# Kernel tuning notes

Measured on AMD Instinct MI355X. Metric: run time of the kernel, lower is better.

The kernel has to match this reference:

```python
import jax, jax.numpy as jnp
import numpy as np

N = 200_000      # total nodes
E = 3_200_000    # directed edges
F = 128          # input features
G = 2_000        # graphs in batch
SIZES = (128, 128, 128, 128, 128, 64)
K = 2            # TAGConv hops
EPS = 1e-5


def setup_inputs() -> dict:
    key = jax.random.key(0)
    ks = jax.random.split(key, 12)
    x = jax.random.normal(ks[0], (N, F), jnp.float32)
    edge_index = jax.random.randint(ks[1], (2, E), 0, N, dtype=jnp.int32).astype(jnp.int64)
    segment_ids = jnp.sort(jax.random.randint(ks[2], (N,), 0, G, dtype=jnp.int32)).astype(jnp.int64)
    conv_W = jax.random.normal(ks[3], (5, (K + 1) * 128, 128), jnp.float32) * 0.05
    conv_W_last = jax.random.normal(ks[4], ((K + 1) * 128, 64), jnp.float32) * 0.05
    bn_gamma = jnp.ones((5, 128), jnp.float32)
    bn_beta = jnp.zeros((5, 128), jnp.float32)
    bn_gamma_last = jnp.ones((64,), jnp.float32)
    bn_beta_last = jnp.zeros((64,), jnp.float32)
    agg_bn_gamma = jnp.ones((4,), jnp.float32)
    agg_bn_beta = jnp.zeros((4,), jnp.float32)
    agg_W = jax.random.normal(ks[5], (64, 4 * 64), jnp.float32) * 0.05
    agg_b = jnp.zeros((64,), jnp.float32)
    out_W = jax.random.normal(ks[6], (1, 64), jnp.float32) * 0.05
    out_b = jnp.zeros((1,), jnp.float32)
    return dict(x=x, edge_index=edge_index, segment_ids=segment_ids, conv_W=conv_W,
                conv_W_last=conv_W_last, bn_gamma=bn_gamma, bn_beta=bn_beta,
                bn_gamma_last=bn_gamma_last, bn_beta_last=bn_beta_last,
                agg_bn_gamma=agg_bn_gamma, agg_bn_beta=agg_bn_beta,
                agg_W=agg_W, agg_b=agg_b, out_W=out_W, out_b=out_b)


def _forward(x, edge_index, segment_ids, conv_W, conv_W_last, bn_gamma, bn_beta,
             bn_gamma_last, bn_beta_last, agg_bn_gamma, agg_bn_beta,
             agg_W, agg_b, out_W, out_b):
    src, dst = edge_index[0], edge_index[1]
    deg = jax.ops.segment_sum(jnp.ones((E,), x.dtype), dst, num_segments=N)
    norm = jnp.where(deg > 0, jax.lax.rsqrt(jnp.maximum(deg, 1.0)), 0.0)[:, None]  # D^{-1/2}

    def prop(h):  # h: [N, d] -> D^{-1/2} A D^{-1/2} h
        return norm * jax.ops.segment_sum((h * norm)[src], dst, num_segments=N)

    def tagconv(h, W):  # concat of A_norm^k h for k=0..K, then linear (no bias; BN follows)
        hs = [h]
        for _ in range(K):
            hs.append(prop(hs[-1]))
        return jnp.concatenate(hs, axis=-1) @ W

    def bn(h, g, b):  # training-mode batchnorm over nodes
        m = h.mean(0)
        v = h.var(0)
        return (h - m) * jax.lax.rsqrt(v + EPS) * g + b

    outs = []
    h = x
    for l in range(len(SIZES)):
        if l < 5:
            W, g, b = conv_W[l], bn_gamma[l], bn_beta[l]
        else:
            W, g, b = conv_W_last, bn_gamma_last, bn_beta_last
        h = jax.nn.relu(bn(tagconv(h, W), g, b))
        if l >= 2 and SIZES[l] == SIZES[l - 2]:  # skip connection
            h = h + outs[l - 2]
        outs.append(h)

    # ragged pooling: (max, min, mean, std) per graph
    counts = jax.ops.segment_sum(jnp.ones((N,), h.dtype), segment_ids, num_segments=G)[:, None]
    s = jax.ops.segment_sum(h, segment_ids, num_segments=G)
    mean = s / jnp.maximum(counts, 1.0)
    ssq = jax.ops.segment_sum(h * h, segment_ids, num_segments=G)
    var = (ssq - counts * mean * mean) / jnp.maximum(counts - 1.0, 1.0)  # unbiased like th.std
    std = jnp.sqrt(jnp.maximum(var, 0.0))
    mx = jax.ops.segment_max(h, segment_ids, num_segments=G)
    mn = jax.ops.segment_min(h, segment_ids, num_segments=G)
    pooled = jnp.stack([mx, mn, mean, std], axis=1)  # [G, 4, 64]

    # aggregation BatchNorm1d over the 4 pooling channels (stats over graphs x feat)
    m = pooled.mean(axis=(0, 2))
    v = pooled.var(axis=(0, 2))
    pooled = (pooled - m[None, :, None]) * jax.lax.rsqrt(v + EPS)[None, :, None] \
             * agg_bn_gamma[None, :, None] + agg_bn_beta[None, :, None]

    flat = pooled.reshape(G, 4 * SIZES[-1])
    hg = flat @ agg_W.T + agg_b           # aggregation Linear(256 -> 64)
    return hg @ out_W.T + out_b           # output Linear(64 -> 1), shape [G, 1]


def reference(x, edge_index, segment_ids, conv_W, conv_W_last, bn_gamma, bn_beta,
              bn_gamma_last, bn_beta_last, agg_bn_gamma, agg_bn_beta,
              agg_W, agg_b, out_W, out_b):
    return _forward(x, edge_index, segment_ids, conv_W, conv_W_last, bn_gamma, bn_beta,
                    bn_gamma_last, bn_beta_last, agg_bn_gamma, agg_bn_beta,
                    agg_W, agg_b, out_W, out_b)
```

## Files before the change

kernel.cpp:

```cpp
#include <hip/hip_runtime.h>
#include <cstddef>
#include <cstdint>

#define N_NODES  200000
#define N_EDGES  3200000
#define N_GRAPHS 2000
#define BN_EPS   1e-5f
#define NB       391
#define BSH      9
#define CHUNK    16384

typedef unsigned int   u32;
typedef unsigned short u16;

using short8   = __attribute__((ext_vector_type(8))) short;
using floatx16 = __attribute__((ext_vector_type(16))) float;

__device__ __forceinline__ float bflo(u32 v) { union {u32 i; float f;} c; c.i = v << 16; return c.f; }
__device__ __forceinline__ float bfhi(u32 v) { union {u32 i; float f;} c; c.i = v & 0xffff0000u; return c.f; }
__device__ __forceinline__ float bf1(u16 v)  { union {u32 i; float f;} c; c.i = ((u32)v) << 16; return c.f; }
__device__ __forceinline__ u32 f2bf(float f) {
    union {float f; u32 i;} c; c.f = f;
    return (c.i + 0x7fffu + ((c.i >> 16) & 1u)) >> 16;
}
__device__ __forceinline__ u32 pack2(float a, float b) { return f2bf(a) | (f2bf(b) << 16); }

__global__ void x2bf_kernel(const float* __restrict__ x, u16* __restrict__ xb, int total4) {
    for (int i = blockIdx.x * 256 + threadIdx.x; i < total4; i += gridDim.x * 256) {
        float4 v = ((const float4*)x)[i];
        uint2 o; o.x = pack2(v.x, v.y); o.y = pack2(v.z, v.w);
        ((uint2*)xb)[i] = o;
    }
}

__global__ void wpack_kernel(const float* __restrict__ W, u16* __restrict__ whi,
                             u16* __restrict__ wlo, int K, int DOUT) {
    int tid = blockIdx.x * 256 + threadIdx.x;
    if (tid >= K * DOUT) return;
    int k = tid / DOUT, nn = tid % DOUT;
    float w = W[tid];
    u16 hi = (u16)f2bf(w);
    float rem = w - bf1(hi);
    u16 lo = (u16)f2bf(rem);
    int dst = (k >> 6) * DOUT * 64 + nn * 64 + (k & 63);
    whi[dst] = hi;
    wlo[dst] = lo;
}

__global__ __launch_bounds__(256)
void bucket_hist(const int* __restrict__ edst, int* __restrict__ bcnt, int e) {
    __shared__ int h[NB];
    for (int t = threadIdx.x; t < NB; t += 256) h[t] = 0;
    __syncthreads();
    int base = blockIdx.x * CHUNK;
    int end  = min(base + CHUNK, e);
    for (int i = base + threadIdx.x; i < end; i += 256)
        atomicAdd(&h[edst[i] >> BSH], 1);
    __syncthreads();
    for (int t = threadIdx.x; t < NB; t += 256)
        if (h[t]) atomicAdd(&bcnt[t], h[t]);
}

__global__ void bucket_scan(const int* __restrict__ bcnt, int* __restrict__ bbase,
                            int* __restrict__ bcur) {
    __shared__ int ls[512];
    int t = threadIdx.x;
    int v = (t < NB) ? bcnt[t] : 0;
    ls[t] = v;
    __syncthreads();
    for (int off = 1; off < 512; off <<= 1) {
        int a = (t >= off) ? ls[t - off] : 0;
        __syncthreads();
        ls[t] += a;
        __syncthreads();
    }
    if (t <= NB) {
        int excl = ls[t] - v;
        bbase[t] = excl;
        if (t < NB) bcur[t] = excl;
    }
}

__global__ __launch_bounds__(256)
void bucket_scatter(const int* __restrict__ esrc, const int* __restrict__ edst,
                    int* __restrict__ bcur, uint2* __restrict__ esorted, int e) {
    __shared__ int h[NB], lbase[NB], lcur[NB];
    for (int t = threadIdx.x; t < NB; t += 256) { h[t] = 0; lcur[t] = 0; }
    __syncthreads();
    int base = blockIdx.x * CHUNK;
    int end  = min(base + CHUNK, e);
    for (int i = base + threadIdx.x; i < end; i += 256)
        atomicAdd(&h[edst[i] >> BSH], 1);
    __syncthreads();
    for (int t = threadIdx.x; t < NB; t += 256)
        lbase[t] = h[t] ? atomicAdd(&bcur[t], h[t]) : 0;
    __syncthreads();
    for (int i = base + threadIdx.x; i < end; i += 256) {
        int d = edst[i];
        int b = d >> BSH;
        int p = lbase[b] + atomicAdd(&lcur[b], 1);
        uint2 ed; ed.x = (u32)esrc[i]; ed.y = (u32)d;
        esorted[p] = ed;
    }
}

__global__ __launch_bounds__(256)
void bucket_fill(const uint2* __restrict__ esorted, const int* __restrict__ bbase,
                 int* __restrict__ rowptr, int* __restrict__ csr,
                 float* __restrict__ normv, int n, int e) {
    __shared__ int cnt[512], loc[512], tsum[256];
    const int b = blockIdx.x;
    const int ebeg = bbase[b], eend = bbase[b + 1];
    const int t = threadIdx.x;
    cnt[t] = 0; cnt[t + 256] = 0;
    __syncthreads();
    for (int i = ebeg + t; i < eend; i += 256)
        atomicAdd(&cnt[esorted[i].y & 511], 1);
    __syncthreads();
    int c0 = cnt[2 * t], c1 = cnt[2 * t + 1];
    tsum[t] = c0 + c1;
    __syncthreads();
    for (int off = 1; off < 256; off <<= 1) {
        int a = (t >= off) ? tsum[t - off] : 0;
        __syncthreads();
        tsum[t] += a;
        __syncthreads();
    }
    int excl = tsum[t] - (c0 + c1);
    loc[2 * t] = excl;
    loc[2 * t + 1] = excl + c0;
    __syncthreads();
    for (int j = t; j < 512; j += 256) {
        int node = (b << 9) + j;
        if (node < n) {
            rowptr[node] = ebeg + loc[j];
            int deg = cnt[j];
            normv[node] = (deg > 0) ? rsqrtf((float)deg) : 0.f;
        }
    }
    if (b == 0 && t == 0) rowptr[n] = e;
    __syncthreads();
    for (int j = t; j < 512; j += 256) cnt[j] = loc[j];
    __syncthreads();
    for (int i = ebeg + t; i < eend; i += 256) {
        uint2 ed = esorted[i];
        int slot = ebeg + atomicAdd(&cnt[ed.y & 511], 1);
        csr[slot] = (int)ed.x;
    }
}

__global__ __launch_bounds__(256)
void prop_kernel(const u16* __restrict__ hin, const float* __restrict__ norm,
                 const int* __restrict__ rowptr, const int* __restrict__ csr,
                 u16* __restrict__ pout, int n) {
    int wave = threadIdx.x >> 6;
    int lane = threadIdx.x & 63;
    int node = blockIdx.x * 4 + wave;
    if (node >= n) return;
    const int q = lane >> 4;
    const int f = (lane & 15) * 8;
    int s = rowptr[node], e = rowptr[node + 1];
    float a0 = 0, a1 = 0, a2 = 0, a3 = 0, a4 = 0, a5 = 0, a6 = 0, a7 = 0;
    int i = s + q;
    for (; i + 12 < e; i += 16) {
        int sn0 = csr[i], sn1 = csr[i + 4], sn2 = csr[i + 8], sn3 = csr[i + 12];
        float nw0 = norm[sn0], nw1 = norm[sn1], nw2 = norm[sn2], nw3 = norm[sn3];
        uint4 v0 = *(const uint4*)(hin + (size_t)sn0 * 128 + f);
        uint4 v1 = *(const uint4*)(hin + (size_t)sn1 * 128 + f);
        uint4 v2 = *(const uint4*)(hin + (size_t)sn2 * 128 + f);
        uint4 v3 = *(const uint4*)(hin + (size_t)sn3 * 128 + f);
        a0 += bflo(v0.x) * nw0 + bflo(v1.x) * nw1 + bflo(v2.x) * nw2 + bflo(v3.x) * nw3;
        a1 += bfhi(v0.x) * nw0 + bfhi(v1.x) * nw1 + bfhi(v2.x) * nw2 + bfhi(v3.x) * nw3;
        a2 += bflo(v0.y) * nw0 + bflo(v1.y) * nw1 + bflo(v2.y) * nw2 + bflo(v3.y) * nw3;
        a3 += bfhi(v0.y) * nw0 + bfhi(v1.y) * nw1 + bfhi(v2.y) * nw2 + bfhi(v3.y) * nw3;
        a4 += bflo(v0.z) * nw0 + bflo(v1.z) * nw1 + bflo(v2.z) * nw2 + bflo(v3.z) * nw3;
        a5 += bfhi(v0.z) * nw0 + bfhi(v1.z) * nw1 + bfhi(v2.z) * nw2 + bfhi(v3.z) * nw3;
        a6 += bflo(v0.w) * nw0 + bflo(v1.w) * nw1 + bflo(v2.w) * nw2 + bflo(v3.w) * nw3;
        a7 += bfhi(v0.w) * nw0 + bfhi(v1.w) * nw1 + bfhi(v2.w) * nw2 + bfhi(v3.w) * nw3;
    }
    for (; i < e; i += 4) {
        int sn0 = csr[i];
        float nw0 = norm[sn0];
        uint4 v0 = *(const uint4*)(hin + (size_t)sn0 * 128 + f);
        a0 += bflo(v0.x) * nw0; a1 += bfhi(v0.x) * nw0;
        a2 += bflo(v0.y) * nw0; a3 += bfhi(v0.y) * nw0;
        a4 += bflo(v0.z) * nw0; a5 += bfhi(v0.z) * nw0;
        a6 += bflo(v0.w) * nw0; a7 += bfhi(v0.w) * nw0;
    }
    a0 += __shfl_down(a0, 32, 64); a1 += __shfl_down(a1, 32, 64);
    a2 += __shfl_down(a2, 32, 64); a3 += __shfl_down(a3, 32, 64);
    a4 += __shfl_down(a4, 32, 64); a5 += __shfl_down(a5, 32, 64);
    a6 += __shfl_down(a6, 32, 64); a7 += __shfl_down(a7, 32, 64);
    a0 += __shfl_down(a0, 16, 64); a1 += __shfl_down(a1, 16, 64);
    a2 += __shfl_down(a2, 16, 64); a3 += __shfl_down(a3, 16, 64);
    a4 += __shfl_down(a4, 16, 64); a5 += __shfl_down(a5, 16, 64);
    a6 += __shfl_down(a6, 16, 64); a7 += __shfl_down(a7, 16, 64);
    if (q == 0) {
        float nd = norm[node];
        uint4 o;
        o.x = pack2(a0 * nd, a1 * nd);
        o.y = pack2(a2 * nd, a3 * nd);
        o.z = pack2(a4 * nd, a5 * nd);
        o.w = pack2(a6 * nd, a7 * nd);
        *(uint4*)(pout + (size_t)node * 128 + f) = o;
    }
}

template <int DOUT>
__global__ __launch_bounds__(256)
void gemm_mfma(const u16* __restrict__ A0, const u16* __restrict__ A1,
               const u16* __restrict__ A2, const u16* __restrict__ whi,
               const u16* __restrict__ wlo, u16* __restrict__ outp,
               float* __restrict__ gstats, int n) {
    constexpr int TJ = DOUT / 64;
    constexpr int BELEMS = DOUT * 64;
    __shared__ u16 As[128 * 64];
    __shared__ u16 Bh[BELEMS];
    __shared__ u16 Bl[BELEMS];
    __shared__ float col_s[DOUT];
    __shared__ float col_q[DOUT];

    const int tid  = threadIdx.x;
    const int wave = tid >> 6;
    const int lane = tid & 63;
    const int wrow = wave >> 1;
    const int wcol = wave & 1;
    const int row0 = blockIdx.x * 128;
    const int m    = lane & 31;
    const int half = lane >> 5;

    const u16* mats[3] = {A0, A1, A2};

    floatx16 acc[2][TJ];
#pragma unroll
    for (int ti = 0; ti < 2; ++ti)
#pragma unroll
        for (int tj = 0; tj < TJ; ++tj)
#pragma unroll
            for (int r = 0; r < 16; ++r) acc[ti][tj][r] = 0.f;

    for (int c = 0; c < 6; ++c) {
        const u16* M = mats[c >> 1];
        const int kloc = (c & 1) * 64;
#pragma unroll
        for (int it = 0; it < 4; ++it) {
            int rib  = wave * 32 + it * 8 + (lane >> 3);
            int grow = row0 + rib;
            if (grow >= n) grow = n - 1;
            uint4 v = *(const uint4*)(M + (size_t)grow * 128 + kloc + (lane & 7) * 8);
            int cc = (lane & 7) ^ (rib & 7);
            *(uint4*)&As[rib * 64 + cc * 8] = v;
        }
        {
            const int cbase = c * BELEMS;
#pragma unroll
            for (int j = 0; j < BELEMS / 2048; ++j) {
                int idx  = tid + j * 256;
                int nrow = idx >> 3, seg = idx & 7;
                int dcc  = seg ^ (nrow & 7);
                *(uint4*)&Bh[nrow * 64 + dcc * 8] =
                    *(const uint4*)(whi + cbase + idx * 8);
                *(uint4*)&Bl[nrow * 64 + dcc * 8] =
                    *(const uint4*)(wlo + cbase + idx * 8);
            }
        }
        __syncthreads();
#pragma unroll
        for (int s = 0; s < 4; ++s) {
            const int cc = s * 2 + half;
            short8 a[2], bhf[TJ], blf[TJ];
#pragma unroll
            for (int ti = 0; ti < 2; ++ti) {
                int r = wrow * 64 + ti * 32 + m;
                a[ti] = *(const short8*)&As[r * 64 + ((cc ^ (r & 7)) * 8)];
            }
#pragma unroll
            for (int tj = 0; tj < TJ; ++tj) {
                int rr = wcol * TJ * 32 + tj * 32 + m;
                int off = rr * 64 + ((cc ^ (rr & 7)) * 8);
                bhf[tj] = *(const short8*)&Bh[off];
                blf[tj] = *(const short8*)&Bl[off];
            }
#pragma unroll
            for (int ti = 0; ti < 2; ++ti)
#pragma unroll
                for (int tj = 0; tj < TJ; ++tj) {
                    acc[ti][tj] = __builtin_amdgcn_mfma_f32_32x32x16_bf16(
                        a[ti], bhf[tj], acc[ti][tj], 0, 0, 0);
                    acc[ti][tj] = __builtin_amdgcn_mfma_f32_32x32x16_bf16(
                        a[ti], blf[tj], acc[ti][tj], 0, 0, 0);
                }
        }
        __syncthreads();
    }

    if (tid < DOUT) { col_s[tid] = 0.f; col_q[tid] = 0.f; }
    __syncthreads();
#pragma unroll
    for (int tj = 0; tj < TJ; ++tj) {
        int gcol = (wcol * TJ + tj) * 32 + m;
        float s = 0.f, qq = 0.f;
#pragma unroll
        for (int ti = 0; ti < 2; ++ti)
#pragma unroll
            for (int r = 0; r < 16; ++r) {
                int grow = row0 + wrow * 64 + ti * 32 + (r & 3) + 8 * (r >> 2) + 4 * half;
                if (grow < n) {
                    float v = acc[ti][tj][r];
                    s += v; qq += v * v;
                    outp[(size_t)grow * DOUT + gcol] = (u16)f2bf(v);
                }
            }
        atomicAdd(&col_s[gcol], s);
        atomicAdd(&col_q[gcol], qq);
    }
    __syncthreads();
    if (tid < DOUT) {
        atomicAdd(&gstats[tid], col_s[tid]);
        atomicAdd(&gstats[DOUT + tid], col_q[tid]);
    }
}

__global__ void bn_finalize(float* __restrict__ stats, const float* __restrict__ gamma,
                            const float* __restrict__ beta, int dout, float inv_n) {
    int c = threadIdx.x;
    if (c < dout) {
        float m = stats[c] * inv_n;
        float var = stats[dout + c] * inv_n - m * m;
        float sc = rsqrtf(var + BN_EPS) * gamma[c];
        stats[2 * dout + c] = sc;
        stats[3 * dout + c] = beta[c] - m * sc;
    }
}

template <int DOUT, bool SKIP>
__global__ __launch_bounds__(256)
void bn_apply(u16* __restrict__ h, const float* __restrict__ stats,
              const u16* __restrict__ skip, int total4) {
    constexpr int C4 = DOUT / 4;
    const float* scale = stats + 2 * DOUT;
    const float* shift = stats + 3 * DOUT;
    for (int idx = blockIdx.x * 256 + threadIdx.x; idx < total4; idx += gridDim.x * 256) {
        int c4 = (idx % C4) * 4;
        uint2 u = ((const uint2*)h)[idx];
        float v0 = bflo(u.x), v1 = bfhi(u.x), v2 = bflo(u.y), v3 = bfhi(u.y);
        v0 = fmaxf(fmaf(v0, scale[c4 + 0], shift[c4 + 0]), 0.f);
        v1 = fmaxf(fmaf(v1, scale[c4 + 1], shift[c4 + 1]), 0.f);
        v2 = fmaxf(fmaf(v2, scale[c4 + 2], shift[c4 + 2]), 0.f);
        v3 = fmaxf(fmaf(v3, scale[c4 + 3], shift[c4 + 3]), 0.f);
        if (SKIP) {
            uint2 sk = ((const uint2*)skip)[idx];
            v0 += bflo(sk.x); v1 += bfhi(sk.x); v2 += bflo(sk.y); v3 += bfhi(sk.y);
        }
        uint2 o; o.x = pack2(v0, v1); o.y = pack2(v2, v3);
        ((uint2*)h)[idx] = o;
    }
}

__global__ void gstart_kernel(const int* __restrict__ seg, int* __restrict__ gstart,
                              int n, int g_count) {
    int i = blockIdx.x * 256 + threadIdx.x;
    if (i >= n) return;
    int cur = seg[i];
    if (i == 0) {
        for (int g = 0; g <= cur; ++g) gstart[g] = 0;
    } else {
        int prev = seg[i - 1];
        for (int g = prev + 1; g <= cur; ++g) gstart[g] = i;
    }
    if (i == n - 1) {
        for (int g = cur + 1; g <= g_count; ++g) gstart[g] = n;
    }
}

__global__ __launch_bounds__(256)
void pool_kernel(const u16* __restrict__ h, const int* __restrict__ gstart,
                 float* __restrict__ pooled, int g_count) {
    int wave = threadIdx.x >> 6;
    int lane = threadIdx.x & 63;
    int g = blockIdx.x * 4 + wave;
    if (g >= g_count) return;
    int s = gstart[g], e = gstart[g + 1];
    float mx = -INFINITY, mn = INFINITY, sm = 0.f, sq = 0.f;
    for (int nidx = s; nidx < e; ++nidx) {
        float v = bf1(h[(size_t)nidx * 64 + lane]);
        mx = fmaxf(mx, v);
        mn = fminf(mn, v);
        sm += v;
        sq += v * v;
    }
    float cnt = (float)(e - s);
    float mean = sm / fmaxf(cnt, 1.f);
    float var = (sq - cnt * mean * mean) / fmaxf(cnt - 1.f, 1.f);
    float sd = sqrtf(fmaxf(var, 0.f));
    size_t base = (size_t)g * 256;
    pooled[base + 0 * 64 + lane] = mx;
    pooled[base + 1 * 64 + lane] = mn;
    pooled[base + 2 * 64 + lane] = mean;
    pooled[base + 3 * 64 + lane] = sd;
}

__global__ void agg_stats(const float* __restrict__ pooled, float* __restrict__ aggstat,
                          int g_count) {
    int ch = blockIdx.x;
    int total = g_count * 64;
    float s = 0.f, q = 0.f;
    for (int i = threadIdx.x; i < total; i += 256) {
        int g = i >> 6, f = i & 63;
        float v = pooled[(size_t)g * 256 + ch * 64 + f];
        s += v; q += v * v;
    }
    __shared__ float ls[256], lq[256];
    ls[threadIdx.x] = s; lq[threadIdx.x] = q;
    __syncthreads();
    for (int off = 128; off > 0; off >>= 1) {
        if (threadIdx.x < off) {
            ls[threadIdx.x] += ls[threadIdx.x + off];
            lq[threadIdx.x] += lq[threadIdx.x + off];
        }
        __syncthreads();
    }
    if (threadIdx.x == 0) {
        float inv = 1.f / (float)total;
        float m = ls[0] * inv;
        aggstat[ch * 2 + 0] = m;
        aggstat[ch * 2 + 1] = lq[0] * inv - m * m;
    }
}

__global__ __launch_bounds__(256)
void final_kernel(const float* __restrict__ pooled, const float* __restrict__ aggstat,
                  const float* __restrict__ agg_gamma, const float* __restrict__ agg_beta,
                  const float* __restrict__ aggW, const float* __restrict__ aggb,
                  const float* __restrict__ outW, const float* __restrict__ outb,
                  float* __restrict__ out, int g_count) {
    __shared__ float sflat[4][256];
    int wave = threadIdx.x >> 6;
    int lane = threadIdx.x & 63;
    int g = blockIdx.x * 4 + wave;
    if (g < g_count) {
#pragma unroll
        for (int c = 0; c < 4; ++c) {
            float v = pooled[(size_t)g * 256 + c * 64 + lane];
            float m = aggstat[c * 2], var = aggstat[c * 2 + 1];
            v = (v - m) * rsqrtf(var + BN_EPS) * agg_gamma[c] + agg_beta[c];
            sflat[wave][c * 64 + lane] = v;
        }
    }
    __syncthreads();
    if (g < g_count) {
        float acc = aggb[lane];
        const float* wrow = aggW + lane * 256;
#pragma unroll 8
        for (int i = 0; i < 256; ++i)
            acc = fmaf(sflat[wave][i], wrow[i], acc);
        float t = acc * outW[lane];
        for (int off = 32; off > 0; off >>= 1) t += __shfl_down(t, off, 64);
        if (lane == 0) out[g] = t + outb[0];
    }
}

extern "C" void kernel_launch(void* const* d_in, const int* in_sizes, int n_in,
                              void* d_out, int out_size, void* d_ws, size_t ws_size,
                              hipStream_t stream) {
    const int N = N_NODES, E = N_EDGES, G = N_GRAPHS;

    const float* x           = (const float*)d_in[0];
    const int*   ei          = (const int*)d_in[1];
    const int*   seg         = (const int*)d_in[2];
    const float* conv_W      = (const float*)d_in[3];
    const float* conv_W_last = (const float*)d_in[4];
    const float* bn_g        = (const float*)d_in[5];
    const float* bn_b        = (const float*)d_in[6];
    const float* bn_gl       = (const float*)d_in[7];
    const float* bn_bl       = (const float*)d_in[8];
    const float* agg_g       = (const float*)d_in[9];
    const float* agg_bt      = (const float*)d_in[10];
    const float* aggW        = (const float*)d_in[11];
    const float* aggb        = (const float*)d_in[12];
    const float* outW        = (const float*)d_in[13];
    const float* outb        = (const float*)d_in[14];
    float* out = (float*)d_out;

    const int* esrc = ei;
    const int* edst = ei + E;

    size_t off = 0;
    auto alloc = [&](size_t bytes) -> void* {
        void* p = (char*)d_ws + off;
        off += (bytes + 255) & ~(size_t)255;
        return p;
    };
    float* normv  = (float*)alloc((size_t)N * 4);
    int*   rowptr = (int*)alloc((size_t)(N + 1) * 4);
    int*   csr    = (int*)alloc((size_t)E * 4);
    int*   bcnt   = (int*)alloc((NB + 1) * 4);
    int*   bbase  = (int*)alloc((NB + 1) * 4);
    int*   bcur   = (int*)alloc((NB + 1) * 4);
    int*   gstart = (int*)alloc((size_t)(G + 1) * 4);
    float* stats  = (float*)alloc(4 * 128 * 4);
    float* aggstat= (float*)alloc(8 * 4);
    float* pooled = (float*)alloc((size_t)G * 256 * 4);
    const size_t WPACK = 5 * 384 * 128 + 384 * 64;
    u16*   whip   = (u16*)alloc(WPACK * 2);
    u16*   wlop   = (u16*)alloc(WPACK * 2);
    u16*   ring0  = (u16*)alloc((size_t)N * 128 * 2);
    u16*   ring1  = (u16*)alloc((size_t)N * 128 * 2);
    u16*   ring2  = (u16*)alloc((size_t)N * 128 * 2);
    u16*   p1     = (u16*)alloc((size_t)N * 128 * 2);
    u16*   p2     = (u16*)alloc((size_t)N * 128 * 2);
    u16*   ring[3] = {ring0, ring1, ring2};
    uint2* esorted = (uint2*)p2;

    hipMemsetAsync(bcnt, 0, (NB + 1) * 4, stream);
    const int nchunk = (E + CHUNK - 1) / CHUNK;
    bucket_hist<<<nchunk, 256, 0, stream>>>(edst, bcnt, E);
    bucket_scan<<<1, 512, 0, stream>>>(bcnt, bbase, bcur);
    bucket_scatter<<<nchunk, 256, 0, stream>>>(esrc, edst, bcur, esorted, E);
    bucket_fill<<<NB, 256, 0, stream>>>(esorted, bbase, rowptr, csr, normv, N, E);

    x2bf_kernel<<<2048, 256, 0, stream>>>(x, ring2, N * 128 / 4);

    for (int l = 0; l < 5; ++l)
        wpack_kernel<<<(384 * 128 + 255) / 256, 256, 0, stream>>>(
            conv_W + (size_t)l * 384 * 128, whip + (size_t)l * 384 * 128,
            wlop + (size_t)l * 384 * 128, 384, 128);
    wpack_kernel<<<(384 * 64 + 255) / 256, 256, 0, stream>>>(
        conv_W_last, whip + (size_t)5 * 384 * 128, wlop + (size_t)5 * 384 * 128, 384, 64);

    gstart_kernel<<<(N + 255) / 256, 256, 0, stream>>>(seg, gstart, N, G);

    const u16* h_in = ring2;
    const int gemm_grid = (N + 127) / 128;
    for (int l = 0; l < 6; ++l) {
        const int dout = (l < 5) ? 128 : 64;
        const u16* whi = whip + (size_t)((l < 5) ? l * 384 * 128 : 5 * 384 * 128);
        const u16* wlo = wlop + (size_t)((l < 5) ? l * 384 * 128 : 5 * 384 * 128);
        const float* gamma = (l < 5) ? (bn_g + l * 128) : bn_gl;
        const float* beta  = (l < 5) ? (bn_b + l * 128) : bn_bl;
        u16* outbuf = ring[l % 3];

        prop_kernel<<<(N + 3) / 4, 256, 0, stream>>>(h_in, normv, rowptr, csr, p1, N);
        prop_kernel<<<(N + 3) / 4, 256, 0, stream>>>(p1, normv, rowptr, csr, p2, N);

        hipMemsetAsync(stats, 0, (size_t)2 * dout * 4, stream);
        if (dout == 128)
            gemm_mfma<128><<<gemm_grid, 256, 0, stream>>>(h_in, p1, p2, whi, wlo, outbuf,
                                                          stats, N);
        else
            gemm_mfma<64><<<gemm_grid, 256, 0, stream>>>(h_in, p1, p2, whi, wlo, outbuf,
                                                         stats, N);
        bn_finalize<<<1, 128, 0, stream>>>(stats, gamma, beta, dout, 1.f / (float)N);

        int total4 = N * dout / 4;
        bool has_skip = (l >= 2 && l < 5);
        const u16* skipb = has_skip ? ring[(l - 2) % 3] : nullptr;
        if (dout == 128) {
            if (has_skip)
                bn_apply<128, true><<<8192, 256, 0, stream>>>(outbuf, stats, skipb, total4);
            else
                bn_apply<128, false><<<8192, 256, 0, stream>>>(outbuf, stats, nullptr, total4);
        } else {
            bn_apply<64, false><<<8192, 256, 0, stream>>>(outbuf, stats, nullptr, total4);
        }
        h_in = outbuf;
    }

    pool_kernel<<<(G + 3) / 4, 256, 0, stream>>>(ring[5 % 3], gstart, pooled, G);
    agg_stats<<<4, 256, 0, stream>>>(pooled, aggstat, G);
    final_kernel<<<(G + 3) / 4, 256, 0, stream>>>(pooled, aggstat, agg_g, agg_bt,
                                                  aggW, aggb, outW, outb, out, G);
}
```

Measured before the change: 2.770 ms.

## Fuse BN finalize into apply/pool, prefetch GEMM tiles, pipeline CSR index loads

Merges the six weight-pack launches into one kernel. The BN finalize kernel and the per-layer stats memsets are removed: scale and shift are now computed inside bn_apply (kept in shared memory) and inside pool_kernel, which also absorbs the last layer's BN+ReLU so that pass over the data disappears. The GEMM now register-prefetches the next K-chunk of A and B while the current chunk runs on MFMA, and prop_kernel loads the next group of CSR indices before accumulating the current one. Together these aim to cut launch overhead, one full memory pass, and exposed load latency, at the cost of higher register pressure in the GEMM and prop kernels.

```diff
diff --git a/kernel.cpp b/kernel.cpp
--- a/kernel.cpp
+++ b/kernel.cpp
@@ -33,18 +33,28 @@
     }
 }
 
-__global__ void wpack_kernel(const float* __restrict__ W, u16* __restrict__ whi,
-                             u16* __restrict__ wlo, int K, int DOUT) {
+__global__ void wpack_all(const float* __restrict__ convW, const float* __restrict__ convWlast,
+                          u16* __restrict__ whi, u16* __restrict__ wlo) {
+    const int PER = 384 * 128;
     int tid = blockIdx.x * 256 + threadIdx.x;
-    if (tid >= K * DOUT) return;
-    int k = tid / DOUT, nn = tid % DOUT;
-    float w = W[tid];
+    float w;
+    int dst;
+    if (tid < 5 * PER) {
+        int l = tid / PER, r = tid % PER;
+        int k = r / 128, nn = r % 128;
+        w = convW[tid];
+        dst = l * PER + (k >> 6) * 128 * 64 + nn * 64 + (k & 63);
+    } else {
+        int r = tid - 5 * PER;
+        if (r >= 384 * 64) return;
+        int k = r / 64, nn = r % 64;
+        w = convWlast[r];
+        dst = 5 * PER + (k >> 6) * 64 * 64 + nn * 64 + (k & 63);
+    }
     u16 hi = (u16)f2bf(w);
     float rem = w - bf1(hi);
-    u16 lo = (u16)f2bf(rem);
-    int dst = (k >> 6) * DOUT * 64 + nn * 64 + (k & 63);
     whi[dst] = hi;
-    wlo[dst] = lo;
+    wlo[dst] = (u16)f2bf(rem);
 }
 
 __global__ __launch_bounds__(256)
@@ -162,21 +172,32 @@
     int s = rowptr[node], e = rowptr[node + 1];
     float a0 = 0, a1 = 0, a2 = 0, a3 = 0, a4 = 0, a5 = 0, a6 = 0, a7 = 0;
     int i = s + q;
-    for (; i + 12 < e; i += 16) {
+    if (i + 12 < e) {
         int sn0 = csr[i], sn1 = csr[i + 4], sn2 = csr[i + 8], sn3 = csr[i + 12];
-        float nw0 = norm[sn0], nw1 = norm[sn1], nw2 = norm[sn2], nw3 = norm[sn3];
-        uint4 v0 = *(const uint4*)(hin + (size_t)sn0 * 128 + f);
-        uint4 v1 = *(const uint4*)(hin + (size_t)sn1 * 128 + f);
-        uint4 v2 = *(const uint4*)(hin + (size_t)sn2 * 128 + f);
-        uint4 v3 = *(const uint4*)(hin + (size_t)sn3 * 128 + f);
-        a0 += bflo(v0.x) * nw0 + bflo(v1.x) * nw1 + bflo(v2.x) * nw2 + bflo(v3.x) * nw3;
-        a1 += bfhi(v0.x) * nw0 + bfhi(v1.x) * nw1 + bfhi(v2.x) * nw2 + bfhi(v3.x) * nw3;
-        a2 += bflo(v0.y) * nw0 + bflo(v1.y) * nw1 + bflo(v2.y) * nw2 + bflo(v3.y) * nw3;
-        a3 += bfhi(v0.y) * nw0 + bfhi(v1.y) * nw1 + bfhi(v2.y) * nw2 + bfhi(v3.y) * nw3;
-        a4 += bflo(v0.z) * nw0 + bflo(v1.z) * nw1 + bflo(v2.z) * nw2 + bflo(v3.z) * nw3;
-        a5 += bfhi(v0.z) * nw0 + bfhi(v1.z) * nw1 + bfhi(v2.z) * nw2 + bfhi(v3.z) * nw3;
-        a6 += bflo(v0.w) * nw0 + bflo(v1.w) * nw1 + bflo(v2.w) * nw2 + bflo(v3.w) * nw3;
-        a7 += bfhi(v0.w) * nw0 + bfhi(v1.w) * nw1 + bfhi(v2.w) * nw2 + bfhi(v3.w) * nw3;
+        while (true) {
+            float nw0 = norm[sn0], nw1 = norm[sn1], nw2 = norm[sn2], nw3 = norm[sn3];
+            uint4 v0 = *(const uint4*)(hin + (size_t)sn0 * 128 + f);
+            uint4 v1 = *(const uint4*)(hin + (size_t)sn1 * 128 + f);
+            uint4 v2 = *(const uint4*)(hin + (size_t)sn2 * 128 + f);
+            uint4 v3 = *(const uint4*)(hin + (size_t)sn3 * 128 + f);
+            int ni = i + 16;
+            bool more = (ni + 12 < e);
+            int t0 = 0, t1 = 0, t2 = 0, t3 = 0;
+            if (more) {
+                t0 = csr[ni]; t1 = csr[ni + 4]; t2 = csr[ni + 8]; t3 = csr[ni + 12];
+            }
+            a0 += bflo(v0.x) * nw0 + bflo(v1.x) * nw1 + bflo(v2.x) * nw2 + bflo(v3.x) * nw3;
+            a1 += bfhi(v0.x) * nw0 + bfhi(v1.x) * nw1 + bfhi(v2.x) * nw2 + bfhi(v3.x) * nw3;
+            a2 += bflo(v0.y) * nw0 + bflo(v1.y) * nw1 + bflo(v2.y) * nw2 + bflo(v3.y) * nw3;
+            a3 += bfhi(v0.y) * nw0 + bfhi(v1.y) * nw1 + bfhi(v2.y) * nw2 + bfhi(v3.y) * nw3;
+            a4 += bflo(v0.z) * nw0 + bflo(v1.z) * nw1 + bflo(v2.z) * nw2 + bflo(v3.z) * nw3;
+            a5 += bfhi(v0.z) * nw0 + bfhi(v1.z) * nw1 + bfhi(v2.z) * nw2 + bfhi(v3.z) * nw3;
+            a6 += bflo(v0.w) * nw0 + bflo(v1.w) * nw1 + bflo(v2.w) * nw2 + bflo(v3.w) * nw3;
+            a7 += bfhi(v0.w) * nw0 + bfhi(v1.w) * nw1 + bfhi(v2.w) * nw2 + bfhi(v3.w) * nw3;
+            i = ni;
+            if (!more) break;
+            sn0 = t0; sn1 = t1; sn2 = t2; sn3 = t3;
+        }
     }
     for (; i < e; i += 4) {
         int sn0 = csr[i];
@@ -214,6 +235,7 @@
                float* __restrict__ gstats, int n) {
     constexpr int TJ = DOUT / 64;
     constexpr int BELEMS = DOUT * 64;
+    constexpr int JW = BELEMS / 2048;
     __shared__ u16 As[128 * 64];
     __shared__ u16 Bh[BELEMS];
     __shared__ u16 Bl[BELEMS];
@@ -239,7 +261,8 @@
 #pragma unroll
             for (int r = 0; r < 16; ++r) acc[ti][tj][r] = 0.f;
 
-    for (int c = 0; c < 6; ++c) {
+    uint4 aReg[4], bhReg[JW], blReg[JW];
+    auto loadA = [&](int c) {
         const u16* M = mats[c >> 1];
         const int kloc = (c & 1) * 64;
 #pragma unroll
@@ -247,24 +270,37 @@
             int rib  = wave * 32 + it * 8 + (lane >> 3);
             int grow = row0 + rib;
             if (grow >= n) grow = n - 1;
-            uint4 v = *(const uint4*)(M + (size_t)grow * 128 + kloc + (lane & 7) * 8);
-            int cc = (lane & 7) ^ (rib & 7);
-            *(uint4*)&As[rib * 64 + cc * 8] = v;
-        }
-        {
-            const int cbase = c * BELEMS;
-#pragma unroll
-            for (int j = 0; j < BELEMS / 2048; ++j) {
-                int idx  = tid + j * 256;
-                int nrow = idx >> 3, seg = idx & 7;
-                int dcc  = seg ^ (nrow & 7);
-                *(uint4*)&Bh[nrow * 64 + dcc * 8] =
-                    *(const uint4*)(whi + cbase + idx * 8);
-                *(uint4*)&Bl[nrow * 64 + dcc * 8] =
-                    *(const uint4*)(wlo + cbase + idx * 8);
-            }
+            aReg[it] = *(const uint4*)(M + (size_t)grow * 128 + kloc + (lane & 7) * 8);
+        }
+    };
+    auto loadB = [&](int c) {
+        const int cbase = c * BELEMS;
+#pragma unroll
+        for (int j = 0; j < JW; ++j) {
+            int idx = tid + j * 256;
+            bhReg[j] = *(const uint4*)(whi + cbase + idx * 8);
+            blReg[j] = *(const uint4*)(wlo + cbase + idx * 8);
+        }
+    };
+
+    loadA(0); loadB(0);
+    for (int c = 0; c < 6; ++c) {
+#pragma unroll
+        for (int it = 0; it < 4; ++it) {
+            int rib = wave * 32 + it * 8 + (lane >> 3);
+            int cc  = (lane & 7) ^ (rib & 7);
+            *(uint4*)&As[rib * 64 + cc * 8] = aReg[it];
+        }
+#pragma unroll
+        for (int j = 0; j < JW; ++j) {
+            int idx = tid + j * 256;
+            int nrow = idx >> 3, seg = idx & 7;
+            int dcc  = seg ^ (nrow & 7);
+            *(uint4*)&Bh[nrow * 64 + dcc * 8] = bhReg[j];
+            *(uint4*)&Bl[nrow * 64 + dcc * 8] = blReg[j];
         }
         __syncthreads();
+        if (c < 5) { loadA(c + 1); loadB(c + 1); }
 #pragma unroll
         for (int s = 0; s < 4; ++s) {
             const int cc = s * 2 + half;
@@ -321,33 +357,30 @@
     }
 }
 
-__global__ void bn_finalize(float* __restrict__ stats, const float* __restrict__ gamma,
-                            const float* __restrict__ beta, int dout, float inv_n) {
-    int c = threadIdx.x;
-    if (c < dout) {
-        float m = stats[c] * inv_n;
-        float var = stats[dout + c] * inv_n - m * m;
-        float sc = rsqrtf(var + BN_EPS) * gamma[c];
-        stats[2 * dout + c] = sc;
-        stats[3 * dout + c] = beta[c] - m * sc;
-    }
-}
-
 template <int DOUT, bool SKIP>
 __global__ __launch_bounds__(256)
 void bn_apply(u16* __restrict__ h, const float* __restrict__ stats,
-              const u16* __restrict__ skip, int total4) {
+              const float* __restrict__ gamma, const float* __restrict__ beta,
+              const u16* __restrict__ skip, int total4, float inv_n) {
     constexpr int C4 = DOUT / 4;
-    const float* scale = stats + 2 * DOUT;
-    const float* shift = stats + 3 * DOUT;
+    __shared__ float sh_scale[DOUT], sh_shift[DOUT];
+    if (threadIdx.x < DOUT) {
+        int t = threadIdx.x;
+        float mm = stats[t] * inv_n;
+        float var = stats[DOUT + t] * inv_n - mm * mm;
+        float sc = rsqrtf(var + BN_EPS) * gamma[t];
+        sh_scale[t] = sc;
+        sh_shift[t] = beta[t] - mm * sc;
+    }
+    __syncthreads();
     for (int idx = blockIdx.x * 256 + threadIdx.x; idx < total4; idx += gridDim.x * 256) {
         int c4 = (idx % C4) * 4;
         uint2 u = ((const uint2*)h)[idx];
         float v0 = bflo(u.x), v1 = bfhi(u.x), v2 = bflo(u.y), v3 = bfhi(u.y);
-        v0 = fmaxf(fmaf(v0, scale[c4 + 0], shift[c4 + 0]), 0.f);
-        v1 = fmaxf(fmaf(v1, scale[c4 + 1], shift[c4 + 1]), 0.f);
-        v2 = fmaxf(fmaf(v2, scale[c4 + 2], shift[c4 + 2]), 0.f);
-        v3 = fmaxf(fmaf(v3, scale[c4 + 3], shift[c4 + 3]), 0.f);
+        v0 = fmaxf(fmaf(v0, sh_scale[c4 + 0], sh_shift[c4 + 0]), 0.f);
+        v1 = fmaxf(fmaf(v1, sh_scale[c4 + 1], sh_shift[c4 + 1]), 0.f);
+        v2 = fmaxf(fmaf(v2, sh_scale[c4 + 2], sh_shift[c4 + 2]), 0.f);
+        v3 = fmaxf(fmaf(v3, sh_scale[c4 + 3], sh_shift[c4 + 3]), 0.f);
         if (SKIP) {
             uint2 sk = ((const uint2*)skip)[idx];
             v0 += bflo(sk.x); v1 += bfhi(sk.x); v2 += bflo(sk.y); v3 += bfhi(sk.y);
@@ -374,16 +407,22 @@
 }
 
 __global__ __launch_bounds__(256)
-void pool_kernel(const u16* __restrict__ h, const int* __restrict__ gstart,
-                 float* __restrict__ pooled, int g_count) {
+void pool_kernel(const u16* __restrict__ hraw, const float* __restrict__ stats,
+                 const float* __restrict__ gamma, const float* __restrict__ beta,
+                 const int* __restrict__ gstart, float* __restrict__ pooled,
+                 int g_count, float inv_n) {
     int wave = threadIdx.x >> 6;
     int lane = threadIdx.x & 63;
     int g = blockIdx.x * 4 + wave;
     if (g >= g_count) return;
+    float mmean = stats[lane] * inv_n;
+    float var = stats[64 + lane] * inv_n - mmean * mmean;
+    float sc = rsqrtf(var + BN_EPS) * gamma[lane];
+    float sh = beta[lane] - mmean * sc;
     int s = gstart[g], e = gstart[g + 1];
     float mx = -INFINITY, mn = INFINITY, sm = 0.f, sq = 0.f;
     for (int nidx = s; nidx < e; ++nidx) {
-        float v = bf1(h[(size_t)nidx * 64 + lane]);
+        float v = fmaxf(fmaf(bf1(hraw[(size_t)nidx * 64 + lane]), sc, sh), 0.f);
         mx = fmaxf(mx, v);
         mn = fminf(mn, v);
         sm += v;
@@ -391,8 +430,8 @@
     }
     float cnt = (float)(e - s);
     float mean = sm / fmaxf(cnt, 1.f);
-    float var = (sq - cnt * mean * mean) / fmaxf(cnt - 1.f, 1.f);
-    float sd = sqrtf(fmaxf(var, 0.f));
+    float var2 = (sq - cnt * mean * mean) / fmaxf(cnt - 1.f, 1.f);
+    float sd = sqrtf(fmaxf(var2, 0.f));
     size_t base = (size_t)g * 256;
     pooled[base + 0 * 64 + lane] = mx;
     pooled[base + 1 * 64 + lane] = mn;
@@ -498,7 +537,7 @@
     int*   bbase  = (int*)alloc((NB + 1) * 4);
     int*   bcur   = (int*)alloc((NB + 1) * 4);
     int*   gstart = (int*)alloc((size_t)(G + 1) * 4);
-    float* stats  = (float*)alloc(4 * 128 * 4);
+    float* statsA = (float*)alloc(6 * 256 * 4);
     float* aggstat= (float*)alloc(8 * 4);
     float* pooled = (float*)alloc((size_t)G * 256 * 4);
     const size_t WPACK = 5 * 384 * 128 + 384 * 64;
@@ -513,6 +552,7 @@
     uint2* esorted = (uint2*)p2;
 
     hipMemsetAsync(bcnt, 0, (NB + 1) * 4, stream);
+    hipMemsetAsync(statsA, 0, 6 * 256 * 4, stream);
     const int nchunk = (E + CHUNK - 1) / CHUNK;
     bucket_hist<<<nchunk, 256, 0, stream>>>(edst, bcnt, E);
     bucket_scan<<<1, 512, 0, stream>>>(bcnt, bbase, bcur);
@@ -521,52 +561,49 @@
 
     x2bf_kernel<<<2048, 256, 0, stream>>>(x, ring2, N * 128 / 4);
 
-    for (int l = 0; l < 5; ++l)
-        wpack_kernel<<<(384 * 128 + 255) / 256, 256, 0, stream>>>(
-            conv_W + (size_t)l * 384 * 128, whip + (size_t)l * 384 * 128,
-            wlop + (size_t)l * 384 * 128, 384, 128);
-    wpack_kernel<<<(384 * 64 + 255) / 256, 256, 0, stream>>>(
-        conv_W_last, whip + (size_t)5 * 384 * 128, wlop + (size_t)5 * 384 * 128, 384, 64);
+    wpack_all<<<(5 * 384 * 128 + 384 * 64 + 255) / 256, 256, 0, stream>>>(
+        conv_W, conv_W_last, whip, wlop);
 
     gstart_kernel<<<(N + 255) / 256, 256, 0, stream>>>(seg, gstart, N, G);
 
     const u16* h_in = ring2;
     const int gemm_grid = (N + 127) / 128;
+    const float inv_n = 1.f / (float)N;
     for (int l = 0; l < 6; ++l) {
         const int dout = (l < 5) ? 128 : 64;
         const u16* whi = whip + (size_t)((l < 5) ? l * 384 * 128 : 5 * 384 * 128);
         const u16* wlo = wlop + (size_t)((l < 5) ? l * 384 * 128 : 5 * 384 * 128);
         const float* gamma = (l < 5) ? (bn_g + l * 128) : bn_gl;
         const float* beta  = (l < 5) ? (bn_b + l * 128) : bn_bl;
+        float* stats = statsA + l * 256;
         u16* outbuf = ring[l % 3];
 
         prop_kernel<<<(N + 3) / 4, 256, 0, stream>>>(h_in, normv, rowptr, csr, p1, N);
         prop_kernel<<<(N + 3) / 4, 256, 0, stream>>>(p1, normv, rowptr, csr, p2, N);
 
-        hipMemsetAsync(stats, 0, (size_t)2 * dout * 4, stream);
         if (dout == 128)
             gemm_mfma<128><<<gemm_grid, 256, 0, stream>>>(h_in, p1, p2, whi, wlo, outbuf,
                                                           stats, N);
         else
             gemm_mfma<64><<<gemm_grid, 256, 0, stream>>>(h_in, p1, p2, whi, wlo, outbuf,
                                                          stats, N);
-        bn_finalize<<<1, 128, 0, stream>>>(stats, gamma, beta, dout, 1.f / (float)N);
-
-        int total4 = N * dout / 4;
-        bool has_skip = (l >= 2 && l < 5);
-        const u16* skipb = has_skip ? ring[(l - 2) % 3] : nullptr;
-        if (dout == 128) {
+
+        if (l < 5) {
+            int total4 = N * dout / 4;
+            bool has_skip = (l >= 2);
+            const u16* skipb = has_skip ? ring[(l - 2) % 3] : nullptr;
             if (has_skip)
-                bn_apply<128, true><<<8192, 256, 0, stream>>>(outbuf, stats, skipb, total4);
+                bn_apply<128, true><<<8192, 256, 0, stream>>>(outbuf, stats, gamma, beta,
+                                                              skipb, total4, inv_n);
             else
-                bn_apply<128, false><<<8192, 256, 0, stream>>>(outbuf, stats, nullptr, total4);
-        } else {
-            bn_apply<64, false><<<8192, 256, 0, stream>>>(outbuf, stats, nullptr, total4);
+                bn_apply<128, false><<<8192, 256, 0, stream>>>(outbuf, stats, gamma, beta,
+                                                               nullptr, total4, inv_n);
         }
         h_in = outbuf;
     }
 
-    pool_kernel<<<(G + 3) / 4, 256, 0, stream>>>(ring[5 % 3], gstart, pooled, G);
+    pool_kernel<<<(G + 3) / 4, 256, 0, stream>>>(ring[5 % 3], statsA + 5 * 256,
+                                                 bn_gl, bn_bl, gstart, pooled, G, inv_n);
     agg_stats<<<4, 256, 0, stream>>>(pooled, aggstat, G);
     final_kernel<<<(G + 3) / 4, 256, 0, stream>>>(pooled, aggstat, agg_g, agg_bt,
                                                   aggW, aggb, outW, outb, out, G);
```

New measurement: 3.402 ms. +22.8%, slower.
